# Kernel optimization log

Measured on AMD Instinct MI355X. Metric: run time of the kernel, lower is better.

Reference implementation:

```python
import jax, jax.numpy as jnp
import numpy as np

NUM_HEADS = 4
GROUPS = 16
EPS = 1e-5


def setup_inputs() -> dict:
    key = jax.random.key(0)
    ks = jax.random.split(key, 7)
    b, c, hh, ww = 4, 256, 64, 64
    x = jax.random.normal(ks[0], (b, c, hh, ww), dtype=jnp.float32)
    norm_w = 1.0 + 0.1 * jax.random.normal(ks[1], (c,), dtype=jnp.float32)
    norm_b = 0.1 * jax.random.normal(ks[2], (c,), dtype=jnp.float32)
    qkv_w = jax.random.normal(ks[3], (3 * c, c), dtype=jnp.float32) / np.sqrt(c)
    qkv_b = 0.01 * jax.random.normal(ks[4], (3 * c,), dtype=jnp.float32)
    # NOTE: original zero-inits proj_out; we use random weights so the
    # attention path actually affects the output (kernel correctness test).
    proj_w = jax.random.normal(ks[5], (c, c), dtype=jnp.float32) / np.sqrt(c)
    proj_b = jnp.zeros((c,), dtype=jnp.float32)
    return {"x": x, "norm_w": norm_w, "norm_b": norm_b,
            "qkv_w": qkv_w, "qkv_b": qkv_b,
            "proj_w": proj_w, "proj_b": proj_b}


def _group_norm(x, w, b):
    # x: [B, C, T]; GroupNorm32 computes in fp32 (inputs already fp32)
    B, C, T = x.shape
    xg = x.reshape(B, GROUPS, C // GROUPS, T)
    mean = jnp.mean(xg, axis=(2, 3), keepdims=True)
    var = jnp.var(xg, axis=(2, 3), keepdims=True)
    xn = ((xg - mean) * jax.lax.rsqrt(var + EPS)).reshape(B, C, T)
    return xn * w[None, :, None] + b[None, :, None]


def reference(x, norm_w, norm_b, qkv_w, qkv_b, proj_w, proj_b):
    b, c = x.shape[0], x.shape[1]
    spatial = x.shape[2:]
    x2 = x.reshape(b, c, -1)                       # [B, C, T]
    T = x2.shape[-1]
    normed = _group_norm(x2, norm_w, norm_b)
    qkv = jnp.einsum('oc,bct->bot', qkv_w, normed) + qkv_b[None, :, None]
    # faithful reshape: [B, 3C, T] -> [B*H, 3C/H, T], then split in thirds
    qkv = qkv.reshape(b * NUM_HEADS, (3 * c) // NUM_HEADS, T)
    ch = qkv.shape[1] // 3                         # = C / H
    q, k, v = jnp.split(qkv, 3, axis=1)
    scale = 1.0 / np.sqrt(np.sqrt(ch))
    weight = jnp.einsum('bct,bcs->bts', q * scale, k * scale)
    weight = jax.nn.softmax(weight.astype(jnp.float32), axis=-1).astype(qkv.dtype)
    h = jnp.einsum('bts,bcs->bct', weight, v)      # [B*H, ch, T]
    h = h.reshape(b, c, T)
    h = jnp.einsum('oc,bct->bot', proj_w, h) + proj_b[None, :, None]
    return (x2 + h).reshape(b, c, *spatial)
```

## Files before the change

### kernel.cpp

```cpp
#include <hip/hip_runtime.h>

constexpr int kB  = 4;
constexpr int kC  = 256;
constexpr int kT  = 4096;
constexpr int kG  = 16;
constexpr int kCg = kC / kG;
constexpr int kH  = 4;
constexpr int kCh = kC / kH;
constexpr float kEps = 1e-5f;
constexpr float kQScale = 0.125f * 1.4426950408889634f;

typedef short bf16x8 __attribute__((ext_vector_type(8)));
typedef float f32x4  __attribute__((ext_vector_type(4)));
typedef float f32x16 __attribute__((ext_vector_type(16)));

__device__ inline unsigned short f2bf(float f) {
    union { float f; unsigned u; } v; v.f = f;
    unsigned r = v.u + 0x7fffu + ((v.u >> 16) & 1u);
    return (unsigned short)(r >> 16);
}
__device__ inline unsigned pk2bf(float a, float b) {
    return (unsigned)f2bf(a) | ((unsigned)f2bf(b) << 16);
}
__device__ inline unsigned pk2bf_trunc(float a, float b) {
    return __builtin_amdgcn_perm(__float_as_uint(b), __float_as_uint(a), 0x07060302u);
}
__device__ inline void pls32(unsigned& a, unsigned& b) {
    __asm__("v_permlane32_swap_b32 %0, %1" : "+v"(a), "+v"(b));
}

__global__ __launch_bounds__(256) void prep_kernel(const float* __restrict__ x,
                                                   float* __restrict__ stats,
                                                   const float* __restrict__ qkv_w,
                                                   const float* __restrict__ proj_w,
                                                   unsigned short* __restrict__ wbf) {
    int tid = threadIdx.x;
    if (blockIdx.x >= 64) {
        int gid = (blockIdx.x - 64) * 256 + tid;
        for (int i = gid; i < 65536; i += 128 * 256) {
            float4 v = (i < 49152) ? ((const float4*)qkv_w)[i]
                                   : ((const float4*)proj_w)[i - 49152];
            *(uint2*)&wbf[(size_t)i * 4] = make_uint2(pk2bf(v.x, v.y), pk2bf(v.z, v.w));
        }
        return;
    }
    int bg = blockIdx.x;
    const float4* xp4 = (const float4*)(x + (size_t)bg * (kCg * kT));
    float s = 0.f, q = 0.f;
    #pragma unroll 4
    for (int i = 0; i < (kCg * kT / 4) / 256; ++i) {
        float4 v = xp4[tid + i * 256];
        s += v.x + v.y + v.z + v.w;
        q += v.x * v.x + v.y * v.y + v.z * v.z + v.w * v.w;
    }
    #pragma unroll
    for (int off = 32; off > 0; off >>= 1) {
        s += __shfl_down(s, off);
        q += __shfl_down(q, off);
    }
    __shared__ float rs[4], rq[4];
    int wid = tid >> 6, lane = tid & 63;
    if (lane == 0) { rs[wid] = s; rq[wid] = q; }
    __syncthreads();
    if (tid == 0) {
        float S = rs[0] + rs[1] + rs[2] + rs[3];
        float Q = rq[0] + rq[1] + rq[2] + rq[3];
        const float invN = 1.0f / (float)(kCg * kT);
        float mean = S * invN;
        float var  = Q * invN - mean * mean;
        stats[bg * 2 + 0] = mean;
        stats[bg * 2 + 1] = rsqrtf(var + kEps);
    }
}

__global__ __launch_bounds__(256) void gn_apply_t_kernel(const float* __restrict__ x,
                                                         const float* __restrict__ stats,
                                                         const float* __restrict__ w,
                                                         const float* __restrict__ bias,
                                                         unsigned short* __restrict__ normT) {
    __shared__ float Ls[64][65];
    int t0 = blockIdx.x * 64;
    int c0 = blockIdx.y * 64;
    int b  = blockIdx.z;
    int tid = threadIdx.x;
    #pragma unroll
    for (int p = 0; p < 4; ++p) {
        int idx = tid + p * 256;
        int cl = idx >> 4, t4 = idx & 15;
        int c = c0 + cl;
        int bg = b * kG + (c >> 4);
        float mean = stats[bg * 2 + 0];
        float rstd = stats[bg * 2 + 1];
        float sw = w[c] * rstd;
        float sb = bias[c] - mean * sw;
        float4 v = *(const float4*)&x[((size_t)b * kC + c) * kT + t0 + t4 * 4];
        Ls[t4 * 4 + 0][cl] = v.x * sw + sb;
        Ls[t4 * 4 + 1][cl] = v.y * sw + sb;
        Ls[t4 * 4 + 2][cl] = v.z * sw + sb;
        Ls[t4 * 4 + 3][cl] = v.w * sw + sb;
    }
    __syncthreads();
    {
        int row = tid >> 2, cq = (tid & 3) * 16;
        unsigned tmp[8];
        #pragma unroll
        for (int i = 0; i < 8; ++i)
            tmp[i] = pk2bf(Ls[row][cq + 2 * i], Ls[row][cq + 2 * i + 1]);
        uint4* dst = (uint4*)&normT[((size_t)b * kT + t0 + row) * kC + c0 + cq];
        dst[0] = make_uint4(tmp[0], tmp[1], tmp[2], tmp[3]);
        dst[1] = make_uint4(tmp[4], tmp[5], tmp[6], tmp[7]);
    }
}

__global__ __launch_bounds__(256) void qkv_gemm_kernel(const unsigned short* __restrict__ wbf,
                                                       const float* __restrict__ qkv_b,
                                                       const unsigned short* __restrict__ normT,
                                                       unsigned short* __restrict__ qTg,
                                                       unsigned short* __restrict__ kTg,
                                                       unsigned short* __restrict__ vCg) {
    constexpr int LDK = 72;
    constexpr int LDV = 136;
    __shared__ __align__(16) unsigned short As[64 * LDK];
    __shared__ __align__(16) unsigned short Bs[128 * LDK];

    int t0 = blockIdx.x * 128;
    int m0 = blockIdx.y * 64;
    int b  = blockIdx.z;
    const unsigned short* Ab = wbf + (size_t)m0 * kC;
    const unsigned short* Bb = normT + (size_t)b * kT * kC;

    int tid = threadIdx.x;
    int wave = tid >> 6, lane = tid & 63;
    int ln15 = lane & 15, quad = lane >> 4;
    int wm = wave >> 1, wt = wave & 1;

    f32x4 acc[2][4] = {};

    for (int k0 = 0; k0 < kC; k0 += 64) {
        __syncthreads();
        #pragma unroll
        for (int p = 0; p < 2; ++p) {
            int idx = tid + p * 256;
            int row = idx >> 3, seg = idx & 7;
            *(uint4*)&As[row * LDK + seg * 8] =
                *(const uint4*)&Ab[(size_t)row * kC + k0 + seg * 8];
        }
        #pragma unroll
        for (int p = 0; p < 4; ++p) {
            int idx = tid + p * 256;
            int row = idx >> 3, seg = idx & 7;
            *(uint4*)&Bs[row * LDK + seg * 8] =
                *(const uint4*)&Bb[(size_t)(t0 + row) * kC + k0 + seg * 8];
        }
        __syncthreads();
        #pragma unroll
        for (int ks = 0; ks < 2; ++ks) {
            bf16x8 af[2], bf[4];
            #pragma unroll
            for (int i = 0; i < 2; ++i)
                af[i] = *(bf16x8*)&As[(wm * 32 + i * 16 + ln15) * LDK + ks * 32 + quad * 8];
            #pragma unroll
            for (int j = 0; j < 4; ++j)
                bf[j] = *(bf16x8*)&Bs[(wt * 64 + j * 16 + ln15) * LDK + ks * 32 + quad * 8];
            #pragma unroll
            for (int i = 0; i < 2; ++i)
                #pragma unroll
                for (int j = 0; j < 4; ++j)
                    acc[i][j] = __builtin_amdgcn_mfma_f32_16x16x32_bf16(
                        af[i], bf[j], acc[i][j], 0, 0, 0);
        }
    }

    int type = (m0 % 192) / 64;
    int h = m0 / 192;
    int bh = b * kH + h;
    __syncthreads();
    #pragma unroll
    for (int i = 0; i < 2; ++i) {
        float4 bv = *(const float4*)&qkv_b[m0 + wm * 32 + i * 16 + quad * 4];
        const float* bp = (const float*)&bv;
        #pragma unroll
        for (int j = 0; j < 4; ++j) {
            int tl = wt * 64 + j * 16 + ln15;
            int c = wm * 32 + i * 16 + quad * 4;
            float v0 = acc[i][j][0] + bp[0];
            float v1 = acc[i][j][1] + bp[1];
            float v2 = acc[i][j][2] + bp[2];
            float v3 = acc[i][j][3] + bp[3];
            if (type == 0) {
                v0 *= kQScale; v1 *= kQScale; v2 *= kQScale; v3 *= kQScale;
            }
            if (type != 2) {
                *(uint2*)&Bs[tl * LDK + c] = make_uint2(pk2bf(v0, v1), pk2bf(v2, v3));
            } else {
                Bs[(c + 0) * LDV + tl] = f2bf(v0);
                Bs[(c + 1) * LDV + tl] = f2bf(v1);
                Bs[(c + 2) * LDV + tl] = f2bf(v2);
                Bs[(c + 3) * LDV + tl] = f2bf(v3);
            }
        }
    }
    __syncthreads();
    if (type != 2) {
        unsigned short* base = ((type == 0) ? qTg : kTg) + (size_t)bh * (kT * kCh);
        #pragma unroll
        for (int p = 0; p < 4; ++p) {
            int f = tid + p * 256;
            int ln = f & 31, hif = (f >> 5) & 1, ks = (f >> 6) & 3, tb = f >> 8;
            *(uint4*)&base[((t0 >> 5) + tb) * 2048 + ks * 512 + hif * 256 + ln * 8] =
                *(uint4*)&Bs[(tb * 32 + ln) * LDK + ks * 16 + hif * 8];
        }
    } else {
        unsigned short* base = vCg + (size_t)bh * (kT * kCh);
        #pragma unroll
        for (int p = 0; p < 4; ++p) {
            int f = tid + p * 256;
            int c = f & 63, hif = (f >> 6) & 1, sg = f >> 7;
            *(uint4*)&base[((t0 >> 4) + sg) * 1024 + hif * 512 + c * 8] =
                *(uint4*)&Bs[c * LDV + sg * 16 + hif * 8];
        }
    }
}

__global__ __launch_bounds__(256, 2) void attn_mfma_kernel(const unsigned short* __restrict__ qTg,
                                                           const unsigned short* __restrict__ kTg,
                                                           const unsigned short* __restrict__ vCg,
                                                           unsigned short* __restrict__ attnT) {
    __shared__ float Ored[2][2][32][64];
    __shared__ float Lred[2][2][64];

    int lid = blockIdx.y * 32 + blockIdx.x;
    int wl  = (lid & 7) * 64 + (lid >> 3);
    int bh  = wl >> 5;
    int t0  = (wl & 31) * 128;
    int b = bh >> 2, h = bh & 3;

    int tid = threadIdx.x;
    int wave = tid >> 6, lane = tid & 63;
    int ln31 = lane & 31, hi = lane >> 5;
    int tc = wave & 1;
    int sh = wave >> 1;

    const unsigned short* qb = qTg + (size_t)bh * (kT * kCh);
    const unsigned short* kb = kTg + (size_t)bh * (kT * kCh);
    const unsigned short* vb = vCg + (size_t)bh * (kT * kCh);

    bf16x8 qA[4], qB[4];
    {
        const unsigned short* qp = qb + ((size_t)(t0 >> 5) + tc * 2) * 2048 + hi * 256 + ln31 * 8;
        #pragma unroll
        for (int ks = 0; ks < 4; ++ks) {
            qA[ks] = *(const bf16x8*)(qp + ks * 512);
            qB[ks] = *(const bf16x8*)(qp + 2048 + ks * 512);
        }
    }

    const unsigned short* kbase = kb + (size_t)sh * 131072 + hi * 256 + ln31 * 8;
    const unsigned short* vbase = vb + (size_t)sh * 131072 + hi * 512 + ln31 * 8;

    float lA = 0.f, lB = 0.f;
    f32x16 oA0 = {}, oA1 = {}, oB0 = {}, oB1 = {};
    union PunP { uint4 u; bf16x8 f; };

    auto loadK = [&](bf16x8* kf, int idx) {
        const unsigned short* kp = kbase + (size_t)idx * 2048;
        kf[0] = *(const bf16x8*)(kp);
        kf[1] = *(const bf16x8*)(kp + 512);
        kf[2] = *(const bf16x8*)(kp + 1024);
        kf[3] = *(const bf16x8*)(kp + 1536);
    };
    auto loadV = [&](bf16x8* vf, int idx) {
        const unsigned short* vp = vbase + (size_t)idx * 2048;
        vf[0] = *(const bf16x8*)(vp);
        vf[1] = *(const bf16x8*)(vp + 256);
        vf[2] = *(const bf16x8*)(vp + 1024);
        vf[3] = *(const bf16x8*)(vp + 1280);
    };

    auto sBlock = [&](const bf16x8* kf, f32x16& sA, f32x16& sB) {
        f32x16 a = {}, c = {};
        __builtin_amdgcn_s_setprio(1);
        #pragma unroll
        for (int ks = 0; ks < 4; ++ks) {
            a = __builtin_amdgcn_mfma_f32_32x32x16_bf16(kf[ks], qA[ks], a, 0, 0, 0);
            c = __builtin_amdgcn_mfma_f32_32x32x16_bf16(kf[ks], qB[ks], c, 0, 0, 0);
        }
        __builtin_amdgcn_s_setprio(0);
        sA = a; sB = c;
    };

    auto softmax_pack = [&](const f32x16& s, float& l, bf16x8& f0, bf16x8& f1) {
        unsigned u00, u01, u10, u11, u20, u21, u30, u31;
        {
            float p0 = __builtin_amdgcn_exp2f(s[0]);
            float p1 = __builtin_amdgcn_exp2f(s[1]);
            float p2 = __builtin_amdgcn_exp2f(s[2]);
            float p3 = __builtin_amdgcn_exp2f(s[3]);
            l += (p0 + p1) + (p2 + p3);
            u00 = pk2bf_trunc(p0, p1); u01 = pk2bf_trunc(p2, p3);
        }
        {
            float p0 = __builtin_amdgcn_exp2f(s[4]);
            float p1 = __builtin_amdgcn_exp2f(s[5]);
            float p2 = __builtin_amdgcn_exp2f(s[6]);
            float p3 = __builtin_amdgcn_exp2f(s[7]);
            l += (p0 + p1) + (p2 + p3);
            u10 = pk2bf_trunc(p0, p1); u11 = pk2bf_trunc(p2, p3);
        }
        {
            float p0 = __builtin_amdgcn_exp2f(s[8]);
            float p1 = __builtin_amdgcn_exp2f(s[9]);
            float p2 = __builtin_amdgcn_exp2f(s[10]);
            float p3 = __builtin_amdgcn_exp2f(s[11]);
            l += (p0 + p1) + (p2 + p3);
            u20 = pk2bf_trunc(p0, p1); u21 = pk2bf_trunc(p2, p3);
        }
        {
            float p0 = __builtin_amdgcn_exp2f(s[12]);
            float p1 = __builtin_amdgcn_exp2f(s[13]);
            float p2 = __builtin_amdgcn_exp2f(s[14]);
            float p3 = __builtin_amdgcn_exp2f(s[15]);
            l += (p0 + p1) + (p2 + p3);
            u30 = pk2bf_trunc(p0, p1); u31 = pk2bf_trunc(p2, p3);
        }
        pls32(u00, u10); pls32(u01, u11);
        pls32(u20, u30); pls32(u21, u31);
        PunP P0, P1;
        P0.u = make_uint4(u00, u01, u10, u11);
        P1.u = make_uint4(u20, u21, u30, u31);
        f0 = P0.f; f1 = P1.f;
    };

    auto finishTile = [&](const f32x16& sA, const f32x16& sB, const bf16x8* vf) {
        bf16x8 FA0, FA1, FB0, FB1;
        softmax_pack(sA, lA, FA0, FA1);
        softmax_pack(sB, lB, FB0, FB1);
        __builtin_amdgcn_s_setprio(1);
        oA0 = __builtin_amdgcn_mfma_f32_32x32x16_bf16(vf[0], FA0, oA0, 0, 0, 0);
        oA1 = __builtin_amdgcn_mfma_f32_32x32x16_bf16(vf[1], FA0, oA1, 0, 0, 0);
        oB0 = __builtin_amdgcn_mfma_f32_32x32x16_bf16(vf[0], FB0, oB0, 0, 0, 0);
        oB1 = __builtin_amdgcn_mfma_f32_32x32x16_bf16(vf[1], FB0, oB1, 0, 0, 0);
        oA0 = __builtin_amdgcn_mfma_f32_32x32x16_bf16(vf[2], FA1, oA0, 0, 0, 0);
        oA1 = __builtin_amdgcn_mfma_f32_32x32x16_bf16(vf[3], FA1, oA1, 0, 0, 0);
        oB0 = __builtin_amdgcn_mfma_f32_32x32x16_bf16(vf[2], FB1, oB0, 0, 0, 0);
        oB1 = __builtin_amdgcn_mfma_f32_32x32x16_bf16(vf[3], FB1, oB1, 0, 0, 0);
        __builtin_amdgcn_s_setprio(0);
    };

    bf16x8 K0[4], V0[4], K1[4], V1[4];
    f32x16 sCA, sCB, sNA, sNB;

    loadK(K0, 0); loadV(V0, 0);
    loadK(K1, 1); loadV(V1, 1);
    sBlock(K0, sCA, sCB);

    #pragma unroll 1
    for (int it = 0; it < 62; it += 2) {
        sBlock(K1, sNA, sNB);
        loadK(K0, it + 2);
        finishTile(sCA, sCB, V0);
        loadV(V0, it + 2);
        sCA = sNA; sCB = sNB;
        sBlock(K0, sNA, sNB);
        loadK(K1, it + 3);
        finishTile(sCA, sCB, V1);
        loadV(V1, it + 3);
        sCA = sNA; sCB = sNB;
    }
    sBlock(K1, sNA, sNB);
    finishTile(sCA, sCB, V0);
    finishTile(sNA, sNB, V1);

    lA += __shfl_xor(lA, 32);
    lB += __shfl_xor(lB, 32);

    if (sh == 1) {
        #pragma unroll
        for (int e = 0; e < 16; ++e) {
            Ored[tc][0][e][lane]      = oA0[e];
            Ored[tc][0][16 + e][lane] = oA1[e];
            Ored[tc][1][e][lane]      = oB0[e];
            Ored[tc][1][16 + e][lane] = oB1[e];
        }
        Lred[tc][0][lane] = lA;
        Lred[tc][1][lane] = lB;
    }
    __syncthreads();
    if (sh == 0) {
        #pragma unroll
        for (int e = 0; e < 16; ++e) {
            oA0[e] += Ored[tc][0][e][lane];
            oA1[e] += Ored[tc][0][16 + e][lane];
            oB0[e] += Ored[tc][1][e][lane];
            oB1[e] += Ored[tc][1][16 + e][lane];
        }
        lA += Lred[tc][0][lane];
        lB += Lred[tc][1][lane];
        #pragma unroll
        for (int ch = 0; ch < 2; ++ch) {
            float linv = 1.0f / (ch ? lB : lA);
            int t = t0 + tc * 64 + ch * 32 + ln31;
            #pragma unroll
            for (int ct = 0; ct < 2; ++ct) {
                const f32x16& ao = ch ? (ct ? oB1 : oB0) : (ct ? oA1 : oA0);
                #pragma unroll
                for (int g = 0; g < 4; ++g) {
                    int c = h * kCh + ct * 32 + 8 * g + 4 * hi;
                    float v0 = ao[4 * g + 0] * linv;
                    float v1 = ao[4 * g + 1] * linv;
                    float v2 = ao[4 * g + 2] * linv;
                    float v3 = ao[4 * g + 3] * linv;
                    *(uint2*)&attnT[((size_t)b * kT + t) * kC + c] =
                        make_uint2(pk2bf(v0, v1), pk2bf(v2, v3));
                }
            }
        }
    }
}

__global__ __launch_bounds__(256) void proj_gemm_kernel(const unsigned short* __restrict__ wpbf,
                                                        const float* __restrict__ proj_b,
                                                        const unsigned short* __restrict__ attnT,
                                                        const float* __restrict__ x,
                                                        float* __restrict__ out) {
    constexpr int LDK = 72;
    __shared__ __align__(16) unsigned short As[64 * LDK];
    __shared__ __align__(16) unsigned short Bs[128 * LDK];

    int t0 = blockIdx.x * 128;
    int m0 = blockIdx.y * 64;
    int b  = blockIdx.z;
    const unsigned short* Ab = wpbf + (size_t)m0 * kC;
    const unsigned short* Bb = attnT + (size_t)b * kT * kC;

    int tid = threadIdx.x;
    int wave = tid >> 6, lane = tid & 63;
    int ln15 = lane & 15, quad = lane >> 4;
    int wm = wave >> 1, wt = wave & 1;

    f32x4 acc[2][4] = {};

    for (int k0 = 0; k0 < kC; k0 += 64) {
        __syncthreads();
        #pragma unroll
        for (int p = 0; p < 2; ++p) {
            int idx = tid + p * 256;
            int row = idx >> 3, seg = idx & 7;
            *(uint4*)&As[row * LDK + seg * 8] =
                *(const uint4*)&Ab[(size_t)row * kC + k0 + seg * 8];
        }
        #pragma unroll
        for (int p = 0; p < 4; ++p) {
            int idx = tid + p * 256;
            int row = idx >> 3, seg = idx & 7;
            *(uint4*)&Bs[row * LDK + seg * 8] =
                *(const uint4*)&Bb[(size_t)(t0 + row) * kC + k0 + seg * 8];
        }
        __syncthreads();
        #pragma unroll
        for (int ks = 0; ks < 2; ++ks) {
            bf16x8 af[2], bf[4];
            #pragma unroll
            for (int i = 0; i < 2; ++i)
                af[i] = *(bf16x8*)&As[(wm * 32 + i * 16 + ln15) * LDK + ks * 32 + quad * 8];
            #pragma unroll
            for (int j = 0; j < 4; ++j)
                bf[j] = *(bf16x8*)&Bs[(wt * 64 + j * 16 + ln15) * LDK + ks * 32 + quad * 8];
            #pragma unroll
            for (int i = 0; i < 2; ++i)
                #pragma unroll
                for (int j = 0; j < 4; ++j)
                    acc[i][j] = __builtin_amdgcn_mfma_f32_16x16x32_bf16(
                        af[i], bf[j], acc[i][j], 0, 0, 0);
        }
    }

    #pragma unroll
    for (int i = 0; i < 2; ++i) {
        float4 bv = *(const float4*)&proj_b[m0 + wm * 32 + i * 16 + quad * 4];
        const float* bp = (const float*)&bv;
        #pragma unroll
        for (int j = 0; j < 4; ++j) {
            int t = t0 + wt * 64 + j * 16 + ln15;
            int mbase = m0 + wm * 32 + i * 16 + quad * 4;
            #pragma unroll
            for (int r = 0; r < 4; ++r) {
                size_t off = ((size_t)b * kC + mbase + r) * kT + t;
                out[off] = acc[i][j][r] + bp[r] + x[off];
            }
        }
    }
}

extern "C" void kernel_launch(void* const* d_in, const int* in_sizes, int n_in,
                              void* d_out, int out_size, void* d_ws, size_t ws_size,
                              hipStream_t stream) {
    const float* x      = (const float*)d_in[0];
    const float* norm_w = (const float*)d_in[1];
    const float* norm_b = (const float*)d_in[2];
    const float* qkv_w  = (const float*)d_in[3];
    const float* qkv_b  = (const float*)d_in[4];
    const float* proj_w = (const float*)d_in[5];
    const float* proj_b = (const float*)d_in[6];
    float* out = (float*)d_out;

    float* stats = (float*)d_ws;
    unsigned short* wsbf  = (unsigned short*)((float*)d_ws + 128);
    unsigned short* normT = wsbf;
    unsigned short* wbf   = normT + (size_t)kB * kT * kC;
    unsigned short* qTp   = wbf + 262144;
    unsigned short* kTp   = qTp + (size_t)kB * kH * kT * kCh;
    unsigned short* vCp   = kTp + (size_t)kB * kH * kT * kCh;
    unsigned short* attnT = vCp + (size_t)kB * kH * kT * kCh;
    unsigned short* wpbf  = wbf + 196608;

    prep_kernel<<<192, 256, 0, stream>>>(x, stats, qkv_w, proj_w, wbf);
    gn_apply_t_kernel<<<dim3(kT / 64, kC / 64, kB), 256, 0, stream>>>(
        x, stats, norm_w, norm_b, normT);
    qkv_gemm_kernel<<<dim3(kT / 128, 12, kB), 256, 0, stream>>>(
        wbf, qkv_b, normT, qTp, kTp, vCp);
    attn_mfma_kernel<<<dim3(kT / 128, kB * kH), 256, 0, stream>>>(qTp, kTp, vCp, attnT);
    proj_gemm_kernel<<<dim3(kT / 128, kC / 64, kB), 256, 0, stream>>>(
        wpbf, proj_b, attnT, x, out);
}
```

Before: 200.0 us.

## Drop key-split in attention; each wave handles 64 queries over full key range

The attention kernel no longer splits the key dimension across wave pairs with an LDS reduction. Each of the four waves now owns 64 distinct queries and loops over all 4096 keys, so a block covers 256 queries and the grid shrinks to 256 blocks with occupancy hint 1. This removes the shared-memory partial-sum reduction and barrier, and also drops the s_setprio hints. In exchange it halves the block count to one per CU on the 256-CU MI355X, which halves per-CU wave parallelism and lengthens the serial loop per wave.

```diff
diff --git a/kernel.cpp b/kernel.cpp
--- a/kernel.cpp
+++ b/kernel.cpp
@@ -13,6 +13,8 @@
 typedef short bf16x8 __attribute__((ext_vector_type(8)));
 typedef float f32x4  __attribute__((ext_vector_type(4)));
 typedef float f32x16 __attribute__((ext_vector_type(16)));
+
+union PunP { uint4 u; bf16x8 f; };
 
 __device__ inline unsigned short f2bf(float f) {
     union { float f; unsigned u; } v; v.f = f;
@@ -222,24 +224,19 @@
     }
 }
 
-__global__ __launch_bounds__(256, 2) void attn_mfma_kernel(const unsigned short* __restrict__ qTg,
+__global__ __launch_bounds__(256, 1) void attn_mfma_kernel(const unsigned short* __restrict__ qTg,
                                                            const unsigned short* __restrict__ kTg,
                                                            const unsigned short* __restrict__ vCg,
                                                            unsigned short* __restrict__ attnT) {
-    __shared__ float Ored[2][2][32][64];
-    __shared__ float Lred[2][2][64];
-
-    int lid = blockIdx.y * 32 + blockIdx.x;
-    int wl  = (lid & 7) * 64 + (lid >> 3);
-    int bh  = wl >> 5;
-    int t0  = (wl & 31) * 128;
+    int lid = blockIdx.x;
+    int wl  = (lid & 7) * 32 + (lid >> 3);
+    int bh  = wl >> 4;
+    int t0  = (wl & 15) * 256;
     int b = bh >> 2, h = bh & 3;
 
     int tid = threadIdx.x;
     int wave = tid >> 6, lane = tid & 63;
     int ln31 = lane & 31, hi = lane >> 5;
-    int tc = wave & 1;
-    int sh = wave >> 1;
 
     const unsigned short* qb = qTg + (size_t)bh * (kT * kCh);
     const unsigned short* kb = kTg + (size_t)bh * (kT * kCh);
@@ -247,7 +244,7 @@
 
     bf16x8 qA[4], qB[4];
     {
-        const unsigned short* qp = qb + ((size_t)(t0 >> 5) + tc * 2) * 2048 + hi * 256 + ln31 * 8;
+        const unsigned short* qp = qb + ((size_t)(t0 >> 5) + wave * 2) * 2048 + hi * 256 + ln31 * 8;
         #pragma unroll
         for (int ks = 0; ks < 4; ++ks) {
             qA[ks] = *(const bf16x8*)(qp + ks * 512);
@@ -255,12 +252,11 @@
         }
     }
 
-    const unsigned short* kbase = kb + (size_t)sh * 131072 + hi * 256 + ln31 * 8;
-    const unsigned short* vbase = vb + (size_t)sh * 131072 + hi * 512 + ln31 * 8;
+    const unsigned short* kbase = kb + hi * 256 + ln31 * 8;
+    const unsigned short* vbase = vb + hi * 512 + ln31 * 8;
 
     float lA = 0.f, lB = 0.f;
     f32x16 oA0 = {}, oA1 = {}, oB0 = {}, oB1 = {};
-    union PunP { uint4 u; bf16x8 f; };
 
     auto loadK = [&](bf16x8* kf, int idx) {
         const unsigned short* kp = kbase + (size_t)idx * 2048;
@@ -279,13 +275,11 @@
 
     auto sBlock = [&](const bf16x8* kf, f32x16& sA, f32x16& sB) {
         f32x16 a = {}, c = {};
-        __builtin_amdgcn_s_setprio(1);
         #pragma unroll
         for (int ks = 0; ks < 4; ++ks) {
             a = __builtin_amdgcn_mfma_f32_32x32x16_bf16(kf[ks], qA[ks], a, 0, 0, 0);
             c = __builtin_amdgcn_mfma_f32_32x32x16_bf16(kf[ks], qB[ks], c, 0, 0, 0);
         }
-        __builtin_amdgcn_s_setprio(0);
         sA = a; sB = c;
     };
 
@@ -335,7 +329,6 @@
         bf16x8 FA0, FA1, FB0, FB1;
         softmax_pack(sA, lA, FA0, FA1);
         softmax_pack(sB, lB, FB0, FB1);
-        __builtin_amdgcn_s_setprio(1);
         oA0 = __builtin_amdgcn_mfma_f32_32x32x16_bf16(vf[0], FA0, oA0, 0, 0, 0);
         oA1 = __builtin_amdgcn_mfma_f32_32x32x16_bf16(vf[1], FA0, oA1, 0, 0, 0);
         oB0 = __builtin_amdgcn_mfma_f32_32x32x16_bf16(vf[0], FB0, oB0, 0, 0, 0);
@@ -344,7 +337,6 @@
         oA1 = __builtin_amdgcn_mfma_f32_32x32x16_bf16(vf[3], FA1, oA1, 0, 0, 0);
         oB0 = __builtin_amdgcn_mfma_f32_32x32x16_bf16(vf[2], FB1, oB0, 0, 0, 0);
         oB1 = __builtin_amdgcn_mfma_f32_32x32x16_bf16(vf[3], FB1, oB1, 0, 0, 0);
-        __builtin_amdgcn_s_setprio(0);
     };
 
     bf16x8 K0[4], V0[4], K1[4], V1[4];
@@ -355,7 +347,7 @@
     sBlock(K0, sCA, sCB);
 
     #pragma unroll 1
-    for (int it = 0; it < 62; it += 2) {
+    for (int it = 0; it < 126; it += 2) {
         sBlock(K1, sNA, sNB);
         loadK(K0, it + 2);
         finishTile(sCA, sCB, V0);
@@ -374,45 +366,22 @@
     lA += __shfl_xor(lA, 32);
     lB += __shfl_xor(lB, 32);
 
-    if (sh == 1) {
-        #pragma unroll
-        for (int e = 0; e < 16; ++e) {
-            Ored[tc][0][e][lane]      = oA0[e];
-            Ored[tc][0][16 + e][lane] = oA1[e];
-            Ored[tc][1][e][lane]      = oB0[e];
-            Ored[tc][1][16 + e][lane] = oB1[e];
-        }
-        Lred[tc][0][lane] = lA;
-        Lred[tc][1][lane] = lB;
-    }
-    __syncthreads();
-    if (sh == 0) {
-        #pragma unroll
-        for (int e = 0; e < 16; ++e) {
-            oA0[e] += Ored[tc][0][e][lane];
-            oA1[e] += Ored[tc][0][16 + e][lane];
-            oB0[e] += Ored[tc][1][e][lane];
-            oB1[e] += Ored[tc][1][16 + e][lane];
-        }
-        lA += Lred[tc][0][lane];
-        lB += Lred[tc][1][lane];
-        #pragma unroll
-        for (int ch = 0; ch < 2; ++ch) {
-            float linv = 1.0f / (ch ? lB : lA);
-            int t = t0 + tc * 64 + ch * 32 + ln31;
-            #pragma unroll
-            for (int ct = 0; ct < 2; ++ct) {
-                const f32x16& ao = ch ? (ct ? oB1 : oB0) : (ct ? oA1 : oA0);
-                #pragma unroll
-                for (int g = 0; g < 4; ++g) {
-                    int c = h * kCh + ct * 32 + 8 * g + 4 * hi;
-                    float v0 = ao[4 * g + 0] * linv;
-                    float v1 = ao[4 * g + 1] * linv;
-                    float v2 = ao[4 * g + 2] * linv;
-                    float v3 = ao[4 * g + 3] * linv;
-                    *(uint2*)&attnT[((size_t)b * kT + t) * kC + c] =
-                        make_uint2(pk2bf(v0, v1), pk2bf(v2, v3));
-                }
+    #pragma unroll
+    for (int ch = 0; ch < 2; ++ch) {
+        float linv = 1.0f / (ch ? lB : lA);
+        int t = t0 + wave * 64 + ch * 32 + ln31;
+        #pragma unroll
+        for (int ct = 0; ct < 2; ++ct) {
+            const f32x16& ao = ch ? (ct ? oB1 : oB0) : (ct ? oA1 : oA0);
+            #pragma unroll
+            for (int g = 0; g < 4; ++g) {
+                int c = h * kCh + ct * 32 + 8 * g + 4 * hi;
+                float v0 = ao[4 * g + 0] * linv;
+                float v1 = ao[4 * g + 1] * linv;
+                float v2 = ao[4 * g + 2] * linv;
+                float v3 = ao[4 * g + 3] * linv;
+                *(uint2*)&attnT[((size_t)b * kT + t) * kC + c] =
+                    make_uint2(pk2bf(v0, v1), pk2bf(v2, v3));
             }
         }
     }
@@ -519,7 +488,7 @@
         x, stats, norm_w, norm_b, normT);
     qkv_gemm_kernel<<<dim3(kT / 128, 12, kB), 256, 0, stream>>>(
         wbf, qkv_b, normT, qTp, kTp, vCp);
-    attn_mfma_kernel<<<dim3(kT / 128, kB * kH), 256, 0, stream>>>(qTp, kTp, vCp, attnT);
+    attn_mfma_kernel<<<256, 256, 0, stream>>>(qTp, kTp, vCp, attnT);
     proj_gemm_kernel<<<dim3(kT / 128, kC / 64, kB), 256, 0, stream>>>(
         wpbf, proj_b, attnT, x, out);
 }
```

Result: no change. 198.1 us (-1.0%).
